# Kernel optimization log

Hardware: AMD Instinct MI355X
Metric: run time of the kernel (lower is better)

The kernel has to match this reference:

```python
import jax, jax.numpy as jnp
import numpy as np

B, S1, S2 = 1024, 25, 10          # batch, hop-1 fanout, hop-2 fanout
N, D, H, C = 100000, 256, 128, 64  # n_node, in_dim, per-branch out_dim, n_class


def setup_inputs() -> dict:
    key = jax.random.key(0)
    ks = jax.random.split(key, 10)
    rn = lambda k, shape: jax.random.normal(k, shape, dtype=jnp.float32) * 0.05
    return {
        "ids0": jax.random.randint(ks[0], (B,), 0, N),
        "ids1": jax.random.randint(ks[1], (B * S1,), 0, N),
        "ids2": jax.random.randint(ks[2], (B * S1 * S2,), 0, N),
        "features": jax.random.normal(ks[3], (N, D), dtype=jnp.float32),
        # aggregator layer 1 (in D, out 2H after concat)
        "Wx1": rn(ks[4], (D, H)), "bx1": jnp.zeros((H,), jnp.float32),
        "Wn1": rn(ks[5], (D, H)), "bn1": jnp.zeros((H,), jnp.float32),
        # aggregator layer 2 (in 2H, out 2H)
        "Wx2": rn(ks[6], (2 * H, H)), "bx2": jnp.zeros((H,), jnp.float32),
        "Wn2": rn(ks[7], (2 * H, H)), "bn2": jnp.zeros((H,), jnp.float32),
        # final linear head
        "Wfc": rn(ks[8], (2 * H, C)), "bfc": jnp.zeros((C,), jnp.float32),
    }


def _mean_agg(x, neibs, Wx, bx, Wn, bn, act):
    # neibs: [x_rows * fanout, d] -> mean over fanout, then concat of two linears
    n = neibs.reshape(x.shape[0], -1, neibs.shape[-1]).mean(axis=1)
    out = jnp.concatenate([x @ Wx + bx, n @ Wn + bn], axis=-1)
    return act(out)


def reference(ids0, ids1, ids2, features,
              Wx1, bx1, Wn1, bn1, Wx2, bx2, Wn2, bn2, Wfc, bfc):
    # hop-wise feature gathers (identity prep)
    h0 = features[ids0]   # [B, D]
    h1 = features[ids1]   # [B*S1, D]
    h2 = features[ids2]   # [B*S1*S2, D]
    # layer 1 aggregation (relu), applied to consecutive hop pairs
    g0 = _mean_agg(h0, h1, Wx1, bx1, Wn1, bn1, jax.nn.relu)   # [B, 2H]
    g1 = _mean_agg(h1, h2, Wx1, bx1, Wn1, bn1, jax.nn.relu)   # [B*S1, 2H]
    # layer 2 aggregation (identity activation on last layer)
    f0 = _mean_agg(g0, g1, Wx2, bx2, Wn2, bn2, lambda v: v)   # [B, 2H]
    return f0 @ Wfc + bfc  # [B, C]
```

## Files before the change

### kernel.cpp

```cpp
#include <hip/hip_runtime.h>

#define DD 256
#define HH 128
#define CC 64
#define BB 1024
#define SS1 25
#define SS2 10
#define NN 100000

typedef __attribute__((ext_vector_type(8))) short bf16x8;
typedef __attribute__((ext_vector_type(4))) float f32x4;

__device__ inline unsigned short f2b(float x) {
    union { float f; unsigned u; } v; v.f = x;
    unsigned r = (v.u + 0x7fffu + ((v.u >> 16) & 1u)) >> 16;
    return (unsigned short)r;
}
__device__ inline float b2f(unsigned u16) {
    union { unsigned u; float f; } v; v.u = u16 << 16;
    return v.f;
}

__global__ __launch_bounds__(256)
void prep_w(const float* __restrict__ Wx, const float* __restrict__ Wn,
            unsigned short* __restrict__ Wsw) {
    const int t    = blockIdx.x * 256 + threadIdx.x;
    const int lane = t & 63;
    const int frag = t >> 6;
    const int kc = frag >> 4, nt = frag & 15;
    const int quad = lane >> 4, lr = lane & 15;
    unsigned short v[8];
#pragma unroll
    for (int j = 0; j < 8; ++j) {
        int k = kc * 32 + quad * 8 + j;
        int n = nt * 16 + lr;
        float w = (n < HH) ? Wx[k * HH + n] : Wn[k * HH + (n - HH)];
        v[j] = f2b(w);
    }
    ((uint4*)Wsw)[t] = *(uint4*)v;
}

#define PQ_BLOCKS 512
#define PQ_TILES  (NN / 32)
#define AS 264

__global__ __launch_bounds__(256, 2)
void pq_gemm(const float* __restrict__ feat,
             const unsigned short* __restrict__ Wsw,
             unsigned short* __restrict__ PQb) {
    __shared__ unsigned short sA[2][32 * AS];
    const int t    = threadIdx.x;
    const int w    = t >> 6, lane = t & 63;
    const int quad = lane >> 4, lr = lane & 15;

    bf16x8 B[8][4];
#pragma unroll
    for (int kc = 0; kc < 8; ++kc)
#pragma unroll
        for (int j = 0; j < 4; ++j)
            B[kc][j] = *(const bf16x8*)&Wsw[((kc * 16 + (w * 4 + j)) * 64 + lane) * 8];

    const int srow = t >> 5, sc = t & 31;

    float4 v[8];
    {
        const float* fb = feat + (long)blockIdx.x * 32 * DD + sc * 8;
#pragma unroll
        for (int i = 0; i < 4; ++i) {
            const float4* src = (const float4*)(fb + (long)(i * 8 + srow) * DD);
            v[2 * i]     = src[0];
            v[2 * i + 1] = src[1];
        }
    }

    int c = 0;
#pragma unroll 1
    for (int tile = blockIdx.x; tile < PQ_TILES; tile += PQ_BLOCKS) {
#pragma unroll
        for (int i = 0; i < 4; ++i) {
            int row = i * 8 + srow;
            float4 a = v[2 * i], b = v[2 * i + 1];
            unsigned short w8[8] = { f2b(a.x), f2b(a.y), f2b(a.z), f2b(a.w),
                                     f2b(b.x), f2b(b.y), f2b(b.z), f2b(b.w) };
            *(uint4*)&sA[c][row * AS + sc * 8] = *(uint4*)w8;
        }
        int tn = tile + PQ_BLOCKS;
        if (tn < PQ_TILES) {
            const float* fn = feat + (long)tn * 32 * DD + sc * 8;
#pragma unroll
            for (int i = 0; i < 4; ++i) {
                const float4* src = (const float4*)(fn + (long)(i * 8 + srow) * DD);
                v[2 * i]     = src[0];
                v[2 * i + 1] = src[1];
            }
        }
        __syncthreads();

        f32x4 acc[2][4] = {};
#pragma unroll
        for (int kc = 0; kc < 8; ++kc) {
            bf16x8 a0 = *(const bf16x8*)&sA[c][(lr)      * AS + kc * 32 + quad * 8];
            bf16x8 a1 = *(const bf16x8*)&sA[c][(16 + lr) * AS + kc * 32 + quad * 8];
#pragma unroll
            for (int j = 0; j < 4; ++j) {
                acc[0][j] = __builtin_amdgcn_mfma_f32_16x16x32_bf16(a0, B[kc][j], acc[0][j], 0, 0, 0);
                acc[1][j] = __builtin_amdgcn_mfma_f32_16x16x32_bf16(a1, B[kc][j], acc[1][j], 0, 0, 0);
            }
        }
        __syncthreads();

#pragma unroll
        for (int rt = 0; rt < 2; ++rt)
#pragma unroll
            for (int j = 0; j < 4; ++j) {
                int col = (w * 4 + j) * 16 + lr;
#pragma unroll
                for (int r = 0; r < 4; ++r)
                    sA[c][(rt * 16 + quad * 4 + r) * AS + col] = f2b(acc[rt][j][r]);
            }
        __syncthreads();

#pragma unroll
        for (int i = 0; i < 4; ++i) {
            int id  = i * 256 + t;
            int row = id >> 5, ch = id & 31;
            uint4 d = *(uint4*)&sA[c][row * AS + ch * 8];
            *(uint4*)&PQb[((long)tile * 32 + row) * DD + ch * 8] = d;
        }
        c ^= 1;
    }
}

__global__ __launch_bounds__(256)
void build_g1(const unsigned short* __restrict__ PQb,
              const int* __restrict__ ids1, const int* __restrict__ ids2,
              const float* __restrict__ bx1, const float* __restrict__ bn1,
              unsigned short* __restrict__ g1b) {
    const int wv   = threadIdx.x >> 6;
    const int lane = threadIdx.x & 63;
    const int sub  = lane >> 5, lr = lane & 31;
    const int row  = blockIdx.x * 8 + wv * 2 + sub;

    long xr = (long)ids1[row];
    uint2 xv = *(const uint2*)&PQb[xr * DD + lr * 4];

    int myid = ids2[row * SS2 + (lr % SS2)];
    float4 acc = {0.f, 0.f, 0.f, 0.f};
#pragma unroll
    for (int j = 0; j < SS2; ++j) {
        long nr = (long)__shfl(myid, (lane & 32) + j);
        uint2 nv = *(const uint2*)&PQb[nr * DD + HH + lr * 4];
        acc.x += b2f(nv.x & 0xffff); acc.y += b2f(nv.x >> 16);
        acc.z += b2f(nv.y & 0xffff); acc.w += b2f(nv.y >> 16);
    }
    float4 bx = *(const float4*)&bx1[lr * 4];
    float4 bn = *(const float4*)&bn1[lr * 4];
    float x0 = fmaxf(b2f(xv.x & 0xffff) + bx.x, 0.f);
    float x1 = fmaxf(b2f(xv.x >> 16)    + bx.y, 0.f);
    float x2 = fmaxf(b2f(xv.y & 0xffff) + bx.z, 0.f);
    float x3 = fmaxf(b2f(xv.y >> 16)    + bx.w, 0.f);
    constexpr float inv = 1.f / SS2;
    float n0 = fmaxf(acc.x * inv + bn.x, 0.f);
    float n1 = fmaxf(acc.y * inv + bn.y, 0.f);
    float n2 = fmaxf(acc.z * inv + bn.z, 0.f);
    float n3 = fmaxf(acc.w * inv + bn.w, 0.f);

    uint2 ox = { (unsigned)f2b(x0) | ((unsigned)f2b(x1) << 16),
                 (unsigned)f2b(x2) | ((unsigned)f2b(x3) << 16) };
    uint2 on = { (unsigned)f2b(n0) | ((unsigned)f2b(n1) << 16),
                 (unsigned)f2b(n2) | ((unsigned)f2b(n3) << 16) };
    *(uint2*)&g1b[(long)row * DD + lr * 4]      = ox;
    *(uint2*)&g1b[(long)row * DD + HH + lr * 4] = on;
}

__global__ __launch_bounds__(256)
void build_g0(const unsigned short* __restrict__ PQb,
              const int* __restrict__ ids0, const int* __restrict__ ids1,
              const float* __restrict__ bx1, const float* __restrict__ bn1,
              float* __restrict__ g0) {
    const int wv   = threadIdx.x >> 6;
    const int lane = threadIdx.x & 63;
    const int sub  = lane >> 5, lr = lane & 31;
    const int row  = blockIdx.x * 8 + wv * 2 + sub;

    long xr = (long)ids0[row];
    uint2 xv = *(const uint2*)&PQb[xr * DD + lr * 4];

    int myid = ids1[row * SS1 + (lr % SS1)];
    float4 acc = {0.f, 0.f, 0.f, 0.f};
#pragma unroll 5
    for (int j = 0; j < SS1; ++j) {
        long nr = (long)__shfl(myid, (lane & 32) + j);
        uint2 nv = *(const uint2*)&PQb[nr * DD + HH + lr * 4];
        acc.x += b2f(nv.x & 0xffff); acc.y += b2f(nv.x >> 16);
        acc.z += b2f(nv.y & 0xffff); acc.w += b2f(nv.y >> 16);
    }
    float4 bx = *(const float4*)&bx1[lr * 4];
    float4 bn = *(const float4*)&bn1[lr * 4];
    constexpr float inv = 1.f / SS1;
    float4 xo = { fmaxf(b2f(xv.x & 0xffff) + bx.x, 0.f),
                  fmaxf(b2f(xv.x >> 16)    + bx.y, 0.f),
                  fmaxf(b2f(xv.y & 0xffff) + bx.z, 0.f),
                  fmaxf(b2f(xv.y >> 16)    + bx.w, 0.f) };
    float4 no = { fmaxf(acc.x * inv + bn.x, 0.f),
                  fmaxf(acc.y * inv + bn.y, 0.f),
                  fmaxf(acc.z * inv + bn.z, 0.f),
                  fmaxf(acc.w * inv + bn.w, 0.f) };
    *(float4*)&g0[(long)row * DD + lr * 4]      = xo;
    *(float4*)&g0[(long)row * DD + HH + lr * 4] = no;
}

__global__ __launch_bounds__(256)
void gm_mean(const unsigned short* __restrict__ g1b, float* __restrict__ gm) {
    const int row  = blockIdx.x * 4 + (threadIdx.x >> 6);
    const int lane = threadIdx.x & 63;
    const unsigned short* base = g1b + (long)row * SS1 * DD + lane * 4;
    float4 acc = {0.f, 0.f, 0.f, 0.f};
#pragma unroll 5
    for (int j = 0; j < SS1; ++j) {
        uint2 u = *(const uint2*)(base + (long)j * DD);
        acc.x += b2f(u.x & 0xffff); acc.y += b2f(u.x >> 16);
        acc.z += b2f(u.y & 0xffff); acc.w += b2f(u.y >> 16);
    }
    constexpr float inv = 1.f / SS1;
    float4 o = { acc.x * inv, acc.y * inv, acc.z * inv, acc.w * inv };
    *(float4*)&gm[(long)row * DD + lane * 4] = o;
}

__global__ __launch_bounds__(256)
void agg2(const float* __restrict__ g0, const float* __restrict__ gm,
          const float* __restrict__ Wx, const float* __restrict__ bx,
          const float* __restrict__ Wn, const float* __restrict__ bn,
          float* __restrict__ f0) {
    constexpr int RT = 16;
    __shared__ float A[RT][DD];
    const int r0 = blockIdx.x * RT;
    const int by = blockIdx.y;
    const int t  = threadIdx.x;
    const float* __restrict__ src = by ? gm : g0;
    const float* __restrict__ W   = by ? Wn : Wx;
    const float* __restrict__ bb  = by ? bn : bx;

#pragma unroll
    for (int i = 0; i < 4; ++i) {
        int id = i * 256 + t;
        int r = id >> 6, c4 = (id & 63) * 4;
        *(float4*)&A[r][c4] = *(const float4*)(src + (long)(r0 + r) * DD + c4);
    }
    __syncthreads();

    const int c  = t & 127;
    const int rh = t >> 7;
    float acc[8];
#pragma unroll
    for (int r = 0; r < 8; ++r) acc[r] = 0.f;
#pragma unroll 4
    for (int k = 0; k < DD; ++k) {
        float wv = W[k * HH + c];
#pragma unroll
        for (int r = 0; r < 8; ++r) acc[r] += A[rh * 8 + r][k] * wv;
    }
    const float bias = bb[c];
#pragma unroll
    for (int r = 0; r < 8; ++r)
        f0[(long)(r0 + rh * 8 + r) * DD + by * HH + c] = acc[r] + bias;
}

__global__ __launch_bounds__(256)
void head_kernel(const float* __restrict__ f0, const float* __restrict__ Wfc,
                 const float* __restrict__ bfc, float* __restrict__ out) {
    constexpr int RT = 16;
    __shared__ float aX[RT][DD];
    const int r0 = blockIdx.x * RT;
    const int t  = threadIdx.x;

#pragma unroll
    for (int i = 0; i < 4; ++i) {
        int id = i * 256 + t;
        int r = id >> 6, c4 = (id & 63) * 4;
        *(float4*)&aX[r][c4] = *(const float4*)(f0 + (long)(r0 + r) * DD + c4);
    }
    __syncthreads();

    const int c  = t & (CC - 1);
    const int rg = t >> 6;
    float acc[4];
#pragma unroll
    for (int r = 0; r < 4; ++r) acc[r] = 0.f;
#pragma unroll 4
    for (int k = 0; k < DD; ++k) {
        float wv = Wfc[k * CC + c];
#pragma unroll
        for (int r = 0; r < 4; ++r) acc[r] += aX[rg * 4 + r][k] * wv;
    }
    const float bias = bfc[c];
#pragma unroll
    for (int r = 0; r < 4; ++r)
        out[(long)(r0 + rg * 4 + r) * CC + c] = acc[r] + bias;
}

extern "C" void kernel_launch(void* const* d_in, const int* in_sizes, int n_in,
                              void* d_out, int out_size, void* d_ws, size_t ws_size,
                              hipStream_t stream) {
    const int*   ids0 = (const int*)d_in[0];
    const int*   ids1 = (const int*)d_in[1];
    const int*   ids2 = (const int*)d_in[2];
    const float* feat = (const float*)d_in[3];
    const float* Wx1  = (const float*)d_in[4];
    const float* bx1  = (const float*)d_in[5];
    const float* Wn1  = (const float*)d_in[6];
    const float* bn1  = (const float*)d_in[7];
    const float* Wx2  = (const float*)d_in[8];
    const float* bx2  = (const float*)d_in[9];
    const float* Wn2  = (const float*)d_in[10];
    const float* bn2  = (const float*)d_in[11];
    const float* Wfc  = (const float*)d_in[12];
    const float* bfc  = (const float*)d_in[13];
    float* out = (float*)d_out;

    const long M1 = (long)BB * SS1;
    float* wsf = (float*)d_ws;
    float* g0 = wsf;  wsf += (long)BB * DD;
    float* gm = wsf;  wsf += (long)BB * DD;
    float* f0 = wsf;  wsf += (long)BB * DD;
    unsigned short* PQb = (unsigned short*)wsf;
    unsigned short* g1b = PQb + (long)NN * DD;
    unsigned short* Wsw = g1b + M1 * DD;

    prep_w<<<32, 256, 0, stream>>>(Wx1, Wn1, Wsw);
    pq_gemm<<<PQ_BLOCKS, 256, 0, stream>>>(feat, Wsw, PQb);
    build_g1<<<M1 / 8, 256, 0, stream>>>(PQb, ids1, ids2, bx1, bn1, g1b);
    build_g0<<<BB / 8, 256, 0, stream>>>(PQb, ids0, ids1, bx1, bn1, g0);
    gm_mean<<<BB / 4, 256, 0, stream>>>(g1b, gm);
    agg2<<<dim3(BB / 16, 2), 256, 0, stream>>>(g0, gm, Wx2, bx2, Wn2, bn2, f0);
    head_kernel<<<BB / 16, 256, 0, stream>>>(f0, Wfc, bfc, out);
}
```

Baseline: 262.3 us.

## Fuse gather, mean, layer-2 and head kernels; split pq_gemm LDS buffers

```diff
diff --git a/kernel.cpp b/kernel.cpp
--- a/kernel.cpp
+++ b/kernel.cpp
@@ -48,7 +48,7 @@
 void pq_gemm(const float* __restrict__ feat,
              const unsigned short* __restrict__ Wsw,
              unsigned short* __restrict__ PQb) {
-    __shared__ unsigned short sA[2][32 * AS];
+    __shared__ unsigned short sAO[2][32 * AS];
     const int t    = threadIdx.x;
     const int w    = t >> 6, lane = t & 63;
     const int quad = lane >> 4, lr = lane & 15;
@@ -73,7 +73,6 @@
         }
     }
 
-    int c = 0;
 #pragma unroll 1
     for (int tile = blockIdx.x; tile < PQ_TILES; tile += PQ_BLOCKS) {
 #pragma unroll
@@ -82,7 +81,7 @@
             float4 a = v[2 * i], b = v[2 * i + 1];
             unsigned short w8[8] = { f2b(a.x), f2b(a.y), f2b(a.z), f2b(a.w),
                                      f2b(b.x), f2b(b.y), f2b(b.z), f2b(b.w) };
-            *(uint4*)&sA[c][row * AS + sc * 8] = *(uint4*)w8;
+            *(uint4*)&sAO[0][row * AS + sc * 8] = *(uint4*)w8;
         }
         int tn = tile + PQ_BLOCKS;
         if (tn < PQ_TILES) {
@@ -94,21 +93,20 @@
                 v[2 * i + 1] = src[1];
             }
         }
-        __syncthreads();
+        asm volatile("s_waitcnt lgkmcnt(0)" ::: "memory");
+        __builtin_amdgcn_s_barrier();
 
         f32x4 acc[2][4] = {};
 #pragma unroll
         for (int kc = 0; kc < 8; ++kc) {
-            bf16x8 a0 = *(const bf16x8*)&sA[c][(lr)      * AS + kc * 32 + quad * 8];
-            bf16x8 a1 = *(const bf16x8*)&sA[c][(16 + lr) * AS + kc * 32 + quad * 8];
+            bf16x8 a0 = *(const bf16x8*)&sAO[0][(lr)      * AS + kc * 32 + quad * 8];
+            bf16x8 a1 = *(const bf16x8*)&sAO[0][(16 + lr) * AS + kc * 32 + quad * 8];
 #pragma unroll
             for (int j = 0; j < 4; ++j) {
                 acc[0][j] = __builtin_amdgcn_mfma_f32_16x16x32_bf16(a0, B[kc][j], acc[0][j], 0, 0, 0);
                 acc[1][j] = __builtin_amdgcn_mfma_f32_16x16x32_bf16(a1, B[kc][j], acc[1][j], 0, 0, 0);
             }
         }
-        __syncthreads();
-
 #pragma unroll
         for (int rt = 0; rt < 2; ++rt)
 #pragma unroll
@@ -116,77 +114,96 @@
                 int col = (w * 4 + j) * 16 + lr;
 #pragma unroll
                 for (int r = 0; r < 4; ++r)
-                    sA[c][(rt * 16 + quad * 4 + r) * AS + col] = f2b(acc[rt][j][r]);
+                    sAO[1][(rt * 16 + quad * 4 + r) * AS + col] = f2b(acc[rt][j][r]);
             }
-        __syncthreads();
+        asm volatile("s_waitcnt lgkmcnt(0)" ::: "memory");
+        __builtin_amdgcn_s_barrier();
 
 #pragma unroll
         for (int i = 0; i < 4; ++i) {
             int id  = i * 256 + t;
             int row = id >> 5, ch = id & 31;
-            uint4 d = *(uint4*)&sA[c][row * AS + ch * 8];
+            uint4 d = *(uint4*)&sAO[1][row * AS + ch * 8];
             *(uint4*)&PQb[((long)tile * 32 + row) * DD + ch * 8] = d;
         }
-        c ^= 1;
     }
 }
 
 __global__ __launch_bounds__(256)
-void build_g1(const unsigned short* __restrict__ PQb,
+void build_gm(const unsigned short* __restrict__ PQb,
               const int* __restrict__ ids1, const int* __restrict__ ids2,
               const float* __restrict__ bx1, const float* __restrict__ bn1,
-              unsigned short* __restrict__ g1b) {
-    const int wv   = threadIdx.x >> 6;
-    const int lane = threadIdx.x & 63;
+              float* __restrict__ gm) {
+    __shared__ float sred[8][256];
+    const int i    = blockIdx.x;
+    const int t    = threadIdx.x;
+    const int wv   = t >> 6;
+    const int lane = t & 63;
     const int sub  = lane >> 5, lr = lane & 31;
-    const int row  = blockIdx.x * 8 + wv * 2 + sub;
-
-    long xr = (long)ids1[row];
+    const int slot = wv * 2 + sub;
+
+    const float4 bx = *(const float4*)&bx1[lr * 4];
+    const float4 bn = *(const float4*)&bn1[lr * 4];
+    float4 xs = {0.f, 0.f, 0.f, 0.f}, ns = {0.f, 0.f, 0.f, 0.f};
+
+#pragma unroll
+    for (int it = 0; it < 4; ++it) {
+        int s = slot + it * 8;
+        if (s < SS1) {
+            int row  = i * SS1 + s;
+            long xr  = (long)ids1[row];
+            uint2 xv = *(const uint2*)&PQb[xr * DD + lr * 4];
+            int myid = ids2[row * SS2 + (lr % SS2)];
+            float4 acc = {0.f, 0.f, 0.f, 0.f};
+#pragma unroll
+            for (int j = 0; j < SS2; ++j) {
+                long nr = (long)__shfl(myid, (lane & 32) + j);
+                uint2 nv = *(const uint2*)&PQb[nr * DD + HH + lr * 4];
+                acc.x += b2f(nv.x & 0xffff); acc.y += b2f(nv.x >> 16);
+                acc.z += b2f(nv.y & 0xffff); acc.w += b2f(nv.y >> 16);
+            }
+            constexpr float inv = 1.f / SS2;
+            xs.x += fmaxf(b2f(xv.x & 0xffff) + bx.x, 0.f);
+            xs.y += fmaxf(b2f(xv.x >> 16)    + bx.y, 0.f);
+            xs.z += fmaxf(b2f(xv.y & 0xffff) + bx.z, 0.f);
+            xs.w += fmaxf(b2f(xv.y >> 16)    + bx.w, 0.f);
+            ns.x += fmaxf(acc.x * inv + bn.x, 0.f);
+            ns.y += fmaxf(acc.y * inv + bn.y, 0.f);
+            ns.z += fmaxf(acc.z * inv + bn.z, 0.f);
+            ns.w += fmaxf(acc.w * inv + bn.w, 0.f);
+        }
+    }
+    *(float4*)&sred[slot][lr * 4]      = xs;
+    *(float4*)&sred[slot][HH + lr * 4] = ns;
+    __syncthreads();
+
+    float r = 0.f;
+#pragma unroll
+    for (int k = 0; k < 8; ++k) r += sred[k][t];
+    gm[(long)i * DD + t] = r * (1.f / SS1);
+}
+
+__global__ __launch_bounds__(256)
+void tail_kernel(const unsigned short* __restrict__ PQb,
+                 const int* __restrict__ ids0, const int* __restrict__ ids1,
+                 const float* __restrict__ bx1, const float* __restrict__ bn1,
+                 const float* __restrict__ gm,
+                 const float* __restrict__ Wx2, const float* __restrict__ bx2,
+                 const float* __restrict__ Wn2, const float* __restrict__ bn2,
+                 const float* __restrict__ Wfc, const float* __restrict__ bfc,
+                 float* __restrict__ out) {
+    __shared__ float G[16][DD];
+    __shared__ float F[8][DD];
+    const int r0   = blockIdx.x * 8;
+    const int t    = threadIdx.x;
+    const int wv   = t >> 6, lane = t & 63;
+    const int sub  = lane >> 5, lr = lane & 31;
+    const int row  = wv * 2 + sub;
+    const int grow = r0 + row;
+
+    long xr  = (long)ids0[grow];
     uint2 xv = *(const uint2*)&PQb[xr * DD + lr * 4];
-
-    int myid = ids2[row * SS2 + (lr % SS2)];
-    float4 acc = {0.f, 0.f, 0.f, 0.f};
-#pragma unroll
-    for (int j = 0; j < SS2; ++j) {
-        long nr = (long)__shfl(myid, (lane & 32) + j);
-        uint2 nv = *(const uint2*)&PQb[nr * DD + HH + lr * 4];
-        acc.x += b2f(nv.x & 0xffff); acc.y += b2f(nv.x >> 16);
-        acc.z += b2f(nv.y & 0xffff); acc.w += b2f(nv.y >> 16);
-    }
-    float4 bx = *(const float4*)&bx1[lr * 4];
-    float4 bn = *(const float4*)&bn1[lr * 4];
-    float x0 = fmaxf(b2f(xv.x & 0xffff) + bx.x, 0.f);
-    float x1 = fmaxf(b2f(xv.x >> 16)    + bx.y, 0.f);
-    float x2 = fmaxf(b2f(xv.y & 0xffff) + bx.z, 0.f);
-    float x3 = fmaxf(b2f(xv.y >> 16)    + bx.w, 0.f);
-    constexpr float inv = 1.f / SS2;
-    float n0 = fmaxf(acc.x * inv + bn.x, 0.f);
-    float n1 = fmaxf(acc.y * inv + bn.y, 0.f);
-    float n2 = fmaxf(acc.z * inv + bn.z, 0.f);
-    float n3 = fmaxf(acc.w * inv + bn.w, 0.f);
-
-    uint2 ox = { (unsigned)f2b(x0) | ((unsigned)f2b(x1) << 16),
-                 (unsigned)f2b(x2) | ((unsigned)f2b(x3) << 16) };
-    uint2 on = { (unsigned)f2b(n0) | ((unsigned)f2b(n1) << 16),
-                 (unsigned)f2b(n2) | ((unsigned)f2b(n3) << 16) };
-    *(uint2*)&g1b[(long)row * DD + lr * 4]      = ox;
-    *(uint2*)&g1b[(long)row * DD + HH + lr * 4] = on;
-}
-
-__global__ __launch_bounds__(256)
-void build_g0(const unsigned short* __restrict__ PQb,
-              const int* __restrict__ ids0, const int* __restrict__ ids1,
-              const float* __restrict__ bx1, const float* __restrict__ bn1,
-              float* __restrict__ g0) {
-    const int wv   = threadIdx.x >> 6;
-    const int lane = threadIdx.x & 63;
-    const int sub  = lane >> 5, lr = lane & 31;
-    const int row  = blockIdx.x * 8 + wv * 2 + sub;
-
-    long xr = (long)ids0[row];
-    uint2 xv = *(const uint2*)&PQb[xr * DD + lr * 4];
-
-    int myid = ids1[row * SS1 + (lr % SS1)];
+    int myid = ids1[(long)grow * SS1 + (lr % SS1)];
     float4 acc = {0.f, 0.f, 0.f, 0.f};
 #pragma unroll 5
     for (int j = 0; j < SS1; ++j) {
@@ -195,108 +212,61 @@
         acc.x += b2f(nv.x & 0xffff); acc.y += b2f(nv.x >> 16);
         acc.z += b2f(nv.y & 0xffff); acc.w += b2f(nv.y >> 16);
     }
-    float4 bx = *(const float4*)&bx1[lr * 4];
-    float4 bn = *(const float4*)&bn1[lr * 4];
-    constexpr float inv = 1.f / SS1;
-    float4 xo = { fmaxf(b2f(xv.x & 0xffff) + bx.x, 0.f),
-                  fmaxf(b2f(xv.x >> 16)    + bx.y, 0.f),
-                  fmaxf(b2f(xv.y & 0xffff) + bx.z, 0.f),
-                  fmaxf(b2f(xv.y >> 16)    + bx.w, 0.f) };
-    float4 no = { fmaxf(acc.x * inv + bn.x, 0.f),
-                  fmaxf(acc.y * inv + bn.y, 0.f),
-                  fmaxf(acc.z * inv + bn.z, 0.f),
-                  fmaxf(acc.w * inv + bn.w, 0.f) };
-    *(float4*)&g0[(long)row * DD + lr * 4]      = xo;
-    *(float4*)&g0[(long)row * DD + HH + lr * 4] = no;
-}
-
-__global__ __launch_bounds__(256)
-void gm_mean(const unsigned short* __restrict__ g1b, float* __restrict__ gm) {
-    const int row  = blockIdx.x * 4 + (threadIdx.x >> 6);
-    const int lane = threadIdx.x & 63;
-    const unsigned short* base = g1b + (long)row * SS1 * DD + lane * 4;
-    float4 acc = {0.f, 0.f, 0.f, 0.f};
-#pragma unroll 5
-    for (int j = 0; j < SS1; ++j) {
-        uint2 u = *(const uint2*)(base + (long)j * DD);
-        acc.x += b2f(u.x & 0xffff); acc.y += b2f(u.x >> 16);
-        acc.z += b2f(u.y & 0xffff); acc.w += b2f(u.y >> 16);
-    }
-    constexpr float inv = 1.f / SS1;
-    float4 o = { acc.x * inv, acc.y * inv, acc.z * inv, acc.w * inv };
-    *(float4*)&gm[(long)row * DD + lane * 4] = o;
-}
-
-__global__ __launch_bounds__(256)
-void agg2(const float* __restrict__ g0, const float* __restrict__ gm,
-          const float* __restrict__ Wx, const float* __restrict__ bx,
-          const float* __restrict__ Wn, const float* __restrict__ bn,
-          float* __restrict__ f0) {
-    constexpr int RT = 16;
-    __shared__ float A[RT][DD];
-    const int r0 = blockIdx.x * RT;
-    const int by = blockIdx.y;
-    const int t  = threadIdx.x;
-    const float* __restrict__ src = by ? gm : g0;
-    const float* __restrict__ W   = by ? Wn : Wx;
-    const float* __restrict__ bb  = by ? bn : bx;
-
-#pragma unroll
-    for (int i = 0; i < 4; ++i) {
-        int id = i * 256 + t;
+    {
+        float4 bx = *(const float4*)&bx1[lr * 4];
+        float4 bn = *(const float4*)&bn1[lr * 4];
+        constexpr float inv = 1.f / SS1;
+        float4 xo = { fmaxf(b2f(xv.x & 0xffff) + bx.x, 0.f),
+                      fmaxf(b2f(xv.x >> 16)    + bx.y, 0.f),
+                      fmaxf(b2f(xv.y & 0xffff) + bx.z, 0.f),
+                      fmaxf(b2f(xv.y >> 16)    + bx.w, 0.f) };
+        float4 no = { fmaxf(acc.x * inv + bn.x, 0.f),
+                      fmaxf(acc.y * inv + bn.y, 0.f),
+                      fmaxf(acc.z * inv + bn.z, 0.f),
+                      fmaxf(acc.w * inv + bn.w, 0.f) };
+        *(float4*)&G[row][lr * 4]      = xo;
+        *(float4*)&G[row][HH + lr * 4] = no;
+    }
+#pragma unroll
+    for (int i2 = 0; i2 < 2; ++i2) {
+        int id = i2 * 256 + t;
         int r = id >> 6, c4 = (id & 63) * 4;
-        *(float4*)&A[r][c4] = *(const float4*)(src + (long)(r0 + r) * DD + c4);
+        *(float4*)&G[8 + r][c4] = *(const float4*)(gm + (long)(r0 + r) * DD + c4);
     }
     __syncthreads();
 
     const int c  = t & 127;
     const int rh = t >> 7;
-    float acc[8];
-#pragma unroll
-    for (int r = 0; r < 8; ++r) acc[r] = 0.f;
+#pragma unroll 1
+    for (int by = 0; by < 2; ++by) {
+        const float* __restrict__ W  = by ? Wn2 : Wx2;
+        const float* __restrict__ bb = by ? bn2 : bx2;
+        const int base = by * 8 + rh * 4;
+        float a4[4] = {0.f, 0.f, 0.f, 0.f};
+#pragma unroll 4
+        for (int k = 0; k < DD; ++k) {
+            float wk = W[k * HH + c];
+#pragma unroll
+            for (int r = 0; r < 4; ++r) a4[r] += G[base + r][k] * wk;
+        }
+        const float bias = bb[c];
+#pragma unroll
+        for (int r = 0; r < 4; ++r) F[rh * 4 + r][by * HH + c] = a4[r] + bias;
+    }
+    __syncthreads();
+
+    const int hc = t & (CC - 1);
+    const int rg = t >> 6;
+    float h0 = 0.f, h1 = 0.f;
 #pragma unroll 4
     for (int k = 0; k < DD; ++k) {
-        float wv = W[k * HH + c];
-#pragma unroll
-        for (int r = 0; r < 8; ++r) acc[r] += A[rh * 8 + r][k] * wv;
-    }
-    const float bias = bb[c];
-#pragma unroll
-    for (int r = 0; r < 8; ++r)
-        f0[(long)(r0 + rh * 8 + r) * DD + by * HH + c] = acc[r] + bias;
-}
-
-__global__ __launch_bounds__(256)
-void head_kernel(const float* __restrict__ f0, const float* __restrict__ Wfc,
-                 const float* __restrict__ bfc, float* __restrict__ out) {
-    constexpr int RT = 16;
-    __shared__ float aX[RT][DD];
-    const int r0 = blockIdx.x * RT;
-    const int t  = threadIdx.x;
-
-#pragma unroll
-    for (int i = 0; i < 4; ++i) {
-        int id = i * 256 + t;
-        int r = id >> 6, c4 = (id & 63) * 4;
-        *(float4*)&aX[r][c4] = *(const float4*)(f0 + (long)(r0 + r) * DD + c4);
-    }
-    __syncthreads();
-
-    const int c  = t & (CC - 1);
-    const int rg = t >> 6;
-    float acc[4];
-#pragma unroll
-    for (int r = 0; r < 4; ++r) acc[r] = 0.f;
-#pragma unroll 4
-    for (int k = 0; k < DD; ++k) {
-        float wv = Wfc[k * CC + c];
-#pragma unroll
-        for (int r = 0; r < 4; ++r) acc[r] += aX[rg * 4 + r][k] * wv;
-    }
-    const float bias = bfc[c];
-#pragma unroll
-    for (int r = 0; r < 4; ++r)
-        out[(long)(r0 + rg * 4 + r) * CC + c] = acc[r] + bias;
+        float wk = Wfc[k * CC + hc];
+        h0 += F[rg * 2][k] * wk;
+        h1 += F[rg * 2 + 1][k] * wk;
+    }
+    const float bias = bfc[hc];
+    out[(long)(r0 + rg * 2) * CC + hc]     = h0 + bias;
+    out[(long)(r0 + rg * 2 + 1) * CC + hc] = h1 + bias;
 }
 
 extern "C" void kernel_launch(void* const* d_in, const int* in_sizes, int n_in,
@@ -318,20 +288,14 @@
     const float* bfc  = (const float*)d_in[13];
     float* out = (float*)d_out;
 
-    const long M1 = (long)BB * SS1;
     float* wsf = (float*)d_ws;
-    float* g0 = wsf;  wsf += (long)BB * DD;
     float* gm = wsf;  wsf += (long)BB * DD;
-    float* f0 = wsf;  wsf += (long)BB * DD;
     unsigned short* PQb = (unsigned short*)wsf;
-    unsigned short* g1b = PQb + (long)NN * DD;
-    unsigned short* Wsw = g1b + M1 * DD;
+    unsigned short* Wsw = PQb + (long)NN * DD;
 
     prep_w<<<32, 256, 0, stream>>>(Wx1, Wn1, Wsw);
     pq_gemm<<<PQ_BLOCKS, 256, 0, stream>>>(feat, Wsw, PQb);
-    build_g1<<<M1 / 8, 256, 0, stream>>>(PQb, ids1, ids2, bx1, bn1, g1b);
-    build_g0<<<BB / 8, 256, 0, stream>>>(PQb, ids0, ids1, bx1, bn1, g0);
-    gm_mean<<<BB / 4, 256, 0, stream>>>(g1b, gm);
-    agg2<<<dim3(BB / 16, 2), 256, 0, stream>>>(g0, gm, Wx2, bx2, Wn2, bn2, f0);
-    head_kernel<<<BB / 16, 256, 0, stream>>>(f0, Wfc, bfc, out);
-}
+    build_gm<<<BB, 256, 0, stream>>>(PQb, ids1, ids2, bx1, bn1, gm);
+    tail_kernel<<<BB / 8, 256, 0, stream>>>(PQb, ids0, ids1, bx1, bn1, gm,
+                                            Wx2, bx2, Wn2, bn2, Wfc, bfc, out);
+}
```

Measured after the change: 282.2 us. 1.08x slower.
